# Performance work log

Hardware: AMD Instinct MI355X
Metric: run time of the kernel (lower is better)

## Reference

```python
import jax, jax.numpy as jnp
import numpy as np

N_HEADS = 16
LN_EPS = 1e-5


def setup_inputs() -> dict:
    key = jax.random.key(0)
    k_z, k_qkv, k_proj = jax.random.split(key, 3)
    b, n, dm = 4, 2048, 1024
    z = jax.random.normal(k_z, (b, n, dm), dtype=jnp.float32)
    gamma = jnp.ones((dm,), dtype=jnp.float32)
    beta = jnp.zeros((dm,), dtype=jnp.float32)
    # parameterize Linear weights as (in, out) so y = x @ w (same math as torch x @ W.T)
    w_qkv = jax.random.normal(k_qkv, (dm, 3 * dm), dtype=jnp.float32) * (1.0 / np.sqrt(dm))
    w_proj = jax.random.normal(k_proj, (dm, dm), dtype=jnp.float32) * (1.0 / np.sqrt(dm))
    b_proj = jnp.zeros((dm,), dtype=jnp.float32)
    return {"z": z, "gamma": gamma, "beta": beta, "w_qkv": w_qkv,
            "w_proj": w_proj, "b_proj": b_proj}


def reference(z, gamma, beta, w_qkv, w_proj, b_proj):
    b, n, dm = z.shape
    h = N_HEADS
    d = dm // h
    scaling = jnp.asarray(np.sqrt(dm / h), dtype=z.dtype)

    # LayerNorm over last dim
    mu = jnp.mean(z, axis=-1, keepdims=True)
    var = jnp.mean(jnp.square(z - mu), axis=-1, keepdims=True)
    zn = (z - mu) * jax.lax.rsqrt(var + LN_EPS) * gamma + beta

    qkv = zn @ w_qkv  # [b, n, 3*dm]
    # einops 'b n (h d qkv_n) -> qkv_n b h n d': qkv index is INNERMOST of packed dim
    qkv = qkv.reshape(b, n, h, d, 3)
    q = qkv[..., 0]  # [b, n, h, d]
    k = qkv[..., 1]
    v = qkv[..., 2]

    scores = jnp.einsum('bqhd,bkhd->bhqk', q, k) / scaling  # [b, h, n, n]
    att = jax.nn.softmax(scores, axis=-1)
    out = jnp.einsum('bhqk,bkhd->bqhd', att, v).reshape(b, n, dm)
    out = out @ w_proj + b_proj  # projection (drop_hidden=False); dropout is identity in eval
    return z + out
```

## Files before the change

kernel.cpp:

```cpp
#include <hip/hip_runtime.h>

typedef unsigned short ushort;
typedef unsigned int uint;

typedef __bf16 bf16x8 __attribute__((ext_vector_type(8)));
typedef float floatx4 __attribute__((ext_vector_type(4)));

constexpr int BATCH = 4;
constexpr int SEQ = 2048;
constexpr int DM = 1024;
constexpr int NH = 16;
constexpr int HD = 64;
constexpr int M = BATCH * SEQ;
constexpr int NQKV = 3 * DM;
constexpr float QSCALE = 0.18033688011112042f;

__device__ __forceinline__ ushort f2b(float f) {
    uint x; __builtin_memcpy(&x, &f, 4);
    x += 0x7fffu + ((x >> 16) & 1u);
    return (ushort)(x >> 16);
}

__device__ __forceinline__ void gload16(const ushort* g, ushort* l) {
    __builtin_amdgcn_global_load_lds(
        (const __attribute__((address_space(1))) void*)g,
        (__attribute__((address_space(3))) void*)l, 16, 0, 0);
}

__global__ __launch_bounds__(256) void transpose_cast(
    const float* __restrict__ in, ushort* __restrict__ out, int R, int C) {
    __shared__ ushort tile[64][65];
    int c0 = blockIdx.x * 64, r0 = blockIdx.y * 64;
    int tx = threadIdx.x & 63, ty = threadIdx.x >> 6;
#pragma unroll
    for (int i = 0; i < 64; i += 4)
        tile[i + ty][tx] = f2b(in[(size_t)(r0 + i + ty) * C + c0 + tx]);
    __syncthreads();
#pragma unroll
    for (int i = 0; i < 64; i += 4)
        out[(size_t)(c0 + i + ty) * R + r0 + tx] = tile[tx][i + ty];
}

__global__ __launch_bounds__(256) void ln_kernel(
    const float* __restrict__ z, const float* __restrict__ gamma,
    const float* __restrict__ beta, ushort* __restrict__ zn) {
    int row = blockIdx.x;
    int t = threadIdx.x;
    float4 v = reinterpret_cast<const float4*>(z + (size_t)row * DM)[t];
    float s = v.x + v.y + v.z + v.w;
    float sq = v.x * v.x + v.y * v.y + v.z * v.z + v.w * v.w;
#pragma unroll
    for (int off = 32; off >= 1; off >>= 1) {
        s  += __shfl_xor(s, off);
        sq += __shfl_xor(sq, off);
    }
    __shared__ float red[8];
    int wave = t >> 6;
    if ((t & 63) == 0) { red[wave] = s; red[wave + 4] = sq; }
    __syncthreads();
    s  = red[0] + red[1] + red[2] + red[3];
    sq = red[4] + red[5] + red[6] + red[7];
    float mean = s * (1.f / DM);
    float var  = sq * (1.f / DM) - mean * mean;
    float rstd = rsqrtf(var + 1e-5f);
    float4 g = reinterpret_cast<const float4*>(gamma)[t];
    float4 bt = reinterpret_cast<const float4*>(beta)[t];
    ushort4 o;
    o.x = f2b((v.x - mean) * rstd * g.x + bt.x);
    o.y = f2b((v.y - mean) * rstd * g.y + bt.y);
    o.z = f2b((v.z - mean) * rstd * g.z + bt.z);
    o.w = f2b((v.w - mean) * rstd * g.w + bt.w);
    reinterpret_cast<ushort4*>(zn + (size_t)row * DM)[t] = o;
}

__device__ __forceinline__ void gemm128_core(
    const ushort* __restrict__ A, const ushort* __restrict__ BT,
    int m0, int n0, int t, floatx4 (&acc)[4][4],
    ushort (*As)[32], ushort (*Bs)[32]) {
    int lane = t & 63, w = t >> 6;
    int l16 = lane & 15, quad = lane >> 4;
    int wm = (w >> 1) * 64, wn = (w & 1) * 64;
#pragma unroll
    for (int i = 0; i < 4; i++)
#pragma unroll
        for (int j = 0; j < 4; j++) acc[i][j] = (floatx4){0.f, 0.f, 0.f, 0.f};

    int sr = (w << 4) + (lane >> 2);
    int seg = (((lane & 3) ^ ((sr >> 1) & 3)) << 3);
    const ushort* gA0 = &A [(size_t)(m0 + sr) * DM + seg];
    const ushort* gA1 = &A [(size_t)(m0 + sr + 64) * DM + seg];
    const ushort* gB0 = &BT[(size_t)(n0 + sr) * DM + seg];
    const ushort* gB1 = &BT[(size_t)(n0 + sr + 64) * DM + seg];
    ushort* lA0 = &As[(w << 4)][0];
    ushort* lA1 = &As[64 + (w << 4)][0];
    ushort* lB0 = &Bs[(w << 4)][0];
    ushort* lB1 = &Bs[64 + (w << 4)][0];
    int sw = (l16 >> 1) & 3;

    for (int k0 = 0; k0 < DM; k0 += 32) {
        gload16(gA0 + k0, lA0);
        gload16(gA1 + k0, lA1);
        gload16(gB0 + k0, lB0);
        gload16(gB1 + k0, lB1);
        __syncthreads();
        bf16x8 af[4], bf[4];
#pragma unroll
        for (int i = 0; i < 4; i++)
            af[i] = *reinterpret_cast<const bf16x8*>(&As[wm + i * 16 + l16][(quad ^ sw) << 3]);
#pragma unroll
        for (int j = 0; j < 4; j++)
            bf[j] = *reinterpret_cast<const bf16x8*>(&Bs[wn + j * 16 + l16][(quad ^ sw) << 3]);
#pragma unroll
        for (int i = 0; i < 4; i++)
#pragma unroll
            for (int j = 0; j < 4; j++)
                acc[i][j] = __builtin_amdgcn_mfma_f32_16x16x32_bf16(af[i], bf[j], acc[i][j], 0, 0, 0);
        __syncthreads();
    }
}

__global__ __launch_bounds__(256) void gemm_qkv(
    const ushort* __restrict__ A,
    const ushort* __restrict__ BT,
    ushort* __restrict__ Q, ushort* __restrict__ K, ushort* __restrict__ V) {
    __shared__ ushort As[128][32];
    __shared__ ushort Bs[128][32];
    int t = threadIdx.x;
    int m0 = blockIdx.y * 128, n0 = blockIdx.x * 128;
    floatx4 acc[4][4];
    gemm128_core(A, BT, m0, n0, t, acc, As, Bs);
    int lane = t & 63, w = t >> 6;
    int l16 = lane & 15, quad = lane >> 4;
    int wm = (w >> 1) * 64, wn = (w & 1) * 64;
#pragma unroll
    for (int j = 0; j < 4; j++) {
        int col = n0 + wn + j * 16 + l16;
        int which = col % 3, hd = col / 3;
        int hi = hd >> 6, di = hd & 63;
        ushort* dst = (which == 0) ? Q : (which == 1) ? K : V;
        float scale = (which == 0) ? QSCALE : 1.0f;
#pragma unroll
        for (int i = 0; i < 4; i++) {
#pragma unroll
            for (int r = 0; r < 4; r++) {
                int row = m0 + wm + i * 16 + quad * 4 + r;
                int bb = row >> 11, nn = row & 2047;
                size_t idx = (which == 2)
                    ? ((size_t)(bb * NH + hi) * HD + di) * SEQ + nn
                    : ((size_t)(bb * NH + hi) * SEQ + nn) * HD + di;
                dst[idx] = f2b(acc[i][j][r] * scale);
            }
        }
    }
}

__global__ __launch_bounds__(256) void gemm_proj(
    const ushort* __restrict__ A,
    const ushort* __restrict__ BT,
    const float* __restrict__ bias, const float* __restrict__ z,
    float* __restrict__ out) {
    __shared__ ushort As[128][32];
    __shared__ ushort Bs[128][32];
    int t = threadIdx.x;
    int m0 = blockIdx.y * 128, n0 = blockIdx.x * 128;
    floatx4 acc[4][4];
    gemm128_core(A, BT, m0, n0, t, acc, As, Bs);
    int lane = t & 63, w = t >> 6;
    int l16 = lane & 15, quad = lane >> 4;
    int wm = (w >> 1) * 64, wn = (w & 1) * 64;
#pragma unroll
    for (int j = 0; j < 4; j++) {
        int col = n0 + wn + j * 16 + l16;
        float bz = bias[col];
#pragma unroll
        for (int i = 0; i < 4; i++) {
#pragma unroll
            for (int r = 0; r < 4; r++) {
                int row = m0 + wm + i * 16 + quad * 4 + r;
                out[(size_t)row * DM + col] =
                    acc[i][j][r] + bz + z[(size_t)row * DM + col];
            }
        }
    }
}

__global__ __launch_bounds__(256) void attn_kernel(
    const ushort* __restrict__ Q, const ushort* __restrict__ K,
    const ushort* __restrict__ Vt, ushort* __restrict__ O) {
    __shared__ ushort QsPs[64 * 64];
    __shared__ ushort Ks[2][64 * 64];
    __shared__ ushort Vs[2][64 * 64];
    int t = threadIdx.x;
    int lane = t & 63, w = t >> 6;
    int l16 = lane & 15, quad = lane >> 4;
    int bb = blockIdx.y >> 4, h = blockIdx.y & 15;
    int q0 = blockIdx.x * 64;
    const ushort* Qg = Q  + (size_t)((bb * NH + h) * SEQ + q0) * HD;
    const ushort* Kg = K  + (size_t)((bb * NH + h) * SEQ) * HD;
    const ushort* Vg = Vt + (size_t)((bb * NH + h) * HD) * SEQ;

    int srow = lane >> 3;
    int lseg = (lane & 7) ^ srow;
    int r0 = 8 * w + srow;

    gload16(Qg + (size_t)r0 * HD + lseg * 8,        &QsPs[w * 512]);
    gload16(Qg + (size_t)(32 + r0) * HD + lseg * 8, &QsPs[2048 + w * 512]);
    gload16(Kg + (size_t)r0 * HD + lseg * 8,        &Ks[0][w * 512]);
    gload16(Kg + (size_t)(32 + r0) * HD + lseg * 8, &Ks[0][2048 + w * 512]);
    gload16(Vg + (size_t)r0 * SEQ + lseg * 8,       &Vs[0][w * 512]);
    gload16(Vg + (size_t)(32 + r0) * SEQ + lseg * 8,&Vs[0][2048 + w * 512]);
    __syncthreads();

    int swl = l16 & 7;
    bf16x8 aq0 = *reinterpret_cast<const bf16x8*>(&QsPs[(16 * w + l16) * 64 + ((quad ^ swl) << 3)]);
    bf16x8 aq1 = *reinterpret_cast<const bf16x8*>(&QsPs[(16 * w + l16) * 64 + (((quad + 4) ^ swl) << 3)]);
    ushort* PsRow = &QsPs[(16 * w + l16) * 64];

    bf16x8 bones;
    {
        union { ushort u[8]; bf16x8 v; } cvt;
        ushort one = (l16 == 0) ? (ushort)0x3F80 : (ushort)0;
#pragma unroll
        for (int i = 0; i < 8; i++) cvt.u[i] = one;
        bones = cvt.v;
    }

    floatx4 Oacc[4], lacc = (floatx4){0.f, 0.f, 0.f, 0.f};
#pragma unroll
    for (int tt = 0; tt < 4; tt++) Oacc[tt] = (floatx4){0.f, 0.f, 0.f, 0.f};

    constexpr int NT = SEQ / 64;
    for (int kt = 0; kt < NT; kt++) {
        int cur = kt & 1;
        if (kt + 1 < NT) {
            const ushort* Kn = Kg + (size_t)(kt + 1) * 64 * HD;
            const ushort* Vn = Vg + (size_t)(kt + 1) * 64;
            gload16(Kn + (size_t)r0 * HD + lseg * 8,         &Ks[cur ^ 1][w * 512]);
            gload16(Kn + (size_t)(32 + r0) * HD + lseg * 8,  &Ks[cur ^ 1][2048 + w * 512]);
            gload16(Vn + (size_t)r0 * SEQ + lseg * 8,        &Vs[cur ^ 1][w * 512]);
            gload16(Vn + (size_t)(32 + r0) * SEQ + lseg * 8, &Vs[cur ^ 1][2048 + w * 512]);
        }
        const ushort* Kc = Ks[cur];
        const ushort* Vc = Vs[cur];

        floatx4 sacc[4];
#pragma unroll
        for (int nt = 0; nt < 4; nt++) {
            bf16x8 ak0 = *reinterpret_cast<const bf16x8*>(&Kc[(nt * 16 + l16) * 64 + ((quad ^ swl) << 3)]);
            bf16x8 ak1 = *reinterpret_cast<const bf16x8*>(&Kc[(nt * 16 + l16) * 64 + (((quad + 4) ^ swl) << 3)]);
            floatx4 sv = (floatx4){0.f, 0.f, 0.f, 0.f};
            sv = __builtin_amdgcn_mfma_f32_16x16x32_bf16(ak0, aq0, sv, 0, 0, 0);
            sv = __builtin_amdgcn_mfma_f32_16x16x32_bf16(ak1, aq1, sv, 0, 0, 0);
            sacc[nt] = sv;
        }
#pragma unroll
        for (int nt = 0; nt < 4; nt++) {
            float p0 = __builtin_amdgcn_exp2f(sacc[nt][0]);
            float p1 = __builtin_amdgcn_exp2f(sacc[nt][1]);
            float p2 = __builtin_amdgcn_exp2f(sacc[nt][2]);
            float p3 = __builtin_amdgcn_exp2f(sacc[nt][3]);
            uint b0, b1, b2, b3;
            __builtin_memcpy(&b0, &p0, 4); __builtin_memcpy(&b1, &p1, 4);
            __builtin_memcpy(&b2, &p2, 4); __builtin_memcpy(&b3, &p3, 4);
            uint2 pk;
            pk.x = __builtin_amdgcn_perm(b1, b0, 0x07060302u);
            pk.y = __builtin_amdgcn_perm(b3, b2, 0x07060302u);
            int lseg2 = 2 * nt + (quad >> 1);
            *reinterpret_cast<uint2*>(&PsRow[((lseg2 ^ swl) << 3) + (quad & 1) * 4]) = pk;
        }
#pragma unroll
        for (int ks = 0; ks < 2; ks++) {
            bf16x8 ap = *reinterpret_cast<const bf16x8*>(
                &PsRow[(((4 * ks + quad) ^ swl) << 3)]);
            lacc = __builtin_amdgcn_mfma_f32_16x16x32_bf16(ap, bones, lacc, 0, 0, 0);
#pragma unroll
            for (int tt = 0; tt < 4; tt++) {
                bf16x8 bv = *reinterpret_cast<const bf16x8*>(
                    &Vc[(tt * 16 + l16) * 64 + ((((ks * 4 + quad)) ^ swl) << 3)]);
                Oacc[tt] = __builtin_amdgcn_mfma_f32_16x16x32_bf16(ap, bv, Oacc[tt], 0, 0, 0);
            }
        }
        __syncthreads();
    }
    float lq[4];
#pragma unroll
    for (int j = 0; j < 4; j++) lq[j] = __shfl(lacc[j], quad << 4);

#pragma unroll
    for (int tt = 0; tt < 4; tt++) {
#pragma unroll
        for (int j = 0; j < 4; j++) {
            int n = q0 + w * 16 + quad * 4 + j;
            int dcol = tt * 16 + l16;
            float val = Oacc[tt][j] / lq[j];
            O[(size_t)(bb * SEQ + n) * DM + h * HD + dcol] = f2b(val);
        }
    }
}

extern "C" void kernel_launch(void* const* d_in, const int* in_sizes, int n_in,
                              void* d_out, int out_size, void* d_ws, size_t ws_size,
                              hipStream_t stream) {
    const float* z      = (const float*)d_in[0];
    const float* gamma  = (const float*)d_in[1];
    const float* beta   = (const float*)d_in[2];
    const float* w_qkv  = (const float*)d_in[3];
    const float* w_proj = (const float*)d_in[4];
    const float* b_proj = (const float*)d_in[5];
    float* out = (float*)d_out;

    char* ws = (char*)d_ws;
    const size_t SZ = (size_t)M * DM * sizeof(ushort);
    ushort* zn   = (ushort*)(ws);
    ushort* Qb   = (ushort*)(ws + SZ);
    ushort* Kb   = (ushort*)(ws + 2 * SZ);
    ushort* Vb   = (ushort*)(ws + 3 * SZ);
    ushort* wqT  = (ushort*)(ws + 4 * SZ);
    ushort* wpT  = (ushort*)(ws + 4 * SZ + (size_t)DM * NQKV * sizeof(ushort));
    ushort* Ob = zn;

    dim3 tq(NQKV / 64, DM / 64);
    transpose_cast<<<tq, 256, 0, stream>>>(w_qkv, wqT, DM, NQKV);
    dim3 tp(DM / 64, DM / 64);
    transpose_cast<<<tp, 256, 0, stream>>>(w_proj, wpT, DM, DM);
    ln_kernel<<<M, 256, 0, stream>>>(z, gamma, beta, zn);
    dim3 g1(NQKV / 128, M / 128);
    gemm_qkv<<<g1, 256, 0, stream>>>(zn, wqT, Qb, Kb, Vb);
    dim3 g2(SEQ / 64, BATCH * NH);
    attn_kernel<<<g2, 256, 0, stream>>>(Qb, Kb, Vb, Ob);
    dim3 g3(DM / 128, M / 128);
    gemm_proj<<<g3, 256, 0, stream>>>(Ob, wpT, b_proj, z, out);
}
```

Measured before the change: 327.4 us.

## Permute QKV weight columns so GEMM epilogue writes contiguous Q/K/V tiles via LDS

The QKV weight transpose now reorders output columns so all Q columns come first, then K, then V. Each 128-column GEMM tile therefore maps to a single tensor and a contiguous range of heads. The epilogue stages the accumulator tile in shared memory, transposing it for V, then writes 16-byte vectorized rows. This replaces the old scattered 2-byte stores with their per-element modulo/divide index math. The cost is extra LDS and two barrier-separated passes in the epilogue.

```diff
diff --git a/kernel.cpp b/kernel.cpp
--- a/kernel.cpp
+++ b/kernel.cpp
@@ -39,6 +39,23 @@
 #pragma unroll
     for (int i = 0; i < 64; i += 4)
         out[(size_t)(c0 + i + ty) * R + r0 + tx] = tile[tx][i + ty];
+}
+
+__global__ __launch_bounds__(256) void transpose_cast_qkv(
+    const float* __restrict__ in, ushort* __restrict__ out) {
+    __shared__ ushort tile[64][65];
+    int c0 = blockIdx.x * 64, r0 = blockIdx.y * 64;
+    int tx = threadIdx.x & 63, ty = threadIdx.x >> 6;
+#pragma unroll
+    for (int i = 0; i < 64; i += 4)
+        tile[i + ty][tx] = f2b(in[(size_t)(r0 + i + ty) * NQKV + c0 + tx]);
+    __syncthreads();
+#pragma unroll
+    for (int i = 0; i < 64; i += 4) {
+        int c = c0 + i + ty;
+        int cp = (c % 3) * DM + c / 3;
+        out[(size_t)cp * DM + r0 + tx] = tile[tx][i + ty];
+    }
 }
 
 __global__ __launch_bounds__(256) void ln_kernel(
@@ -125,6 +142,7 @@
     ushort* __restrict__ Q, ushort* __restrict__ K, ushort* __restrict__ V) {
     __shared__ ushort As[128][32];
     __shared__ ushort Bs[128][32];
+    __shared__ ushort Cs[9216];
     int t = threadIdx.x;
     int m0 = blockIdx.y * 128, n0 = blockIdx.x * 128;
     floatx4 acc[4][4];
@@ -132,23 +150,59 @@
     int lane = t & 63, w = t >> 6;
     int l16 = lane & 15, quad = lane >> 4;
     int wm = (w >> 1) * 64, wn = (w & 1) * 64;
-#pragma unroll
-    for (int j = 0; j < 4; j++) {
-        int col = n0 + wn + j * 16 + l16;
-        int which = col % 3, hd = col / 3;
-        int hi = hd >> 6, di = hd & 63;
-        ushort* dst = (which == 0) ? Q : (which == 1) ? K : V;
-        float scale = (which == 0) ? QSCALE : 1.0f;
-#pragma unroll
-        for (int i = 0; i < 4; i++) {
-#pragma unroll
-            for (int r = 0; r < 4; r++) {
-                int row = m0 + wm + i * 16 + quad * 4 + r;
-                int bb = row >> 11, nn = row & 2047;
-                size_t idx = (which == 2)
-                    ? ((size_t)(bb * NH + hi) * HD + di) * SEQ + nn
-                    : ((size_t)(bb * NH + hi) * SEQ + nn) * HD + di;
-                dst[idx] = f2b(acc[i][j][r] * scale);
+    int which = n0 >> 10;
+    int hd0 = n0 & 1023;
+    float scale = (which == 0) ? QSCALE : 1.0f;
+    int bb = m0 >> 11;
+    int nb = m0 & 2047;
+    ushort* dstQK = (which == 0) ? Q : K;
+
+#pragma unroll
+    for (int p = 0; p < 2; p++) {
+        __syncthreads();
+        if ((w >> 1) == p) {
+            if (which < 2) {
+#pragma unroll
+                for (int i = 0; i < 4; i++)
+#pragma unroll
+                    for (int j = 0; j < 4; j++)
+#pragma unroll
+                        for (int r = 0; r < 4; r++)
+                            Cs[(i * 16 + quad * 4 + r) * 136 + wn + j * 16 + l16] =
+                                f2b(acc[i][j][r] * scale);
+            } else {
+#pragma unroll
+                for (int i = 0; i < 4; i++)
+#pragma unroll
+                    for (int j = 0; j < 4; j++)
+#pragma unroll
+                        for (int r = 0; r < 4; r++)
+                            Cs[(wn + j * 16 + l16) * 72 + i * 16 + quad * 4 + r] =
+                                f2b(acc[i][j][r]);
+            }
+        }
+        __syncthreads();
+        if (which < 2) {
+            int ch = (t & 15) * 8;
+#pragma unroll
+            for (int u = 0; u < 4; u++) {
+                int lr = (t >> 4) + u * 16;
+                int n = nb + p * 64 + lr;
+                int hh = (hd0 + ch) >> 6, dd = ch & 63;
+                *reinterpret_cast<uint4*>(
+                    &dstQK[((size_t)((bb * NH + hh) * SEQ) + n) * HD + dd]) =
+                    *reinterpret_cast<const uint4*>(&Cs[lr * 136 + ch]);
+            }
+        } else {
+            int nch = (t & 7) * 8;
+#pragma unroll
+            for (int u = 0; u < 4; u++) {
+                int dc = (t >> 3) + u * 32;
+                int hh = (hd0 >> 6) + (dc >> 6), dd = dc & 63;
+                int n = nb + p * 64 + nch;
+                *reinterpret_cast<uint4*>(
+                    &V[((size_t)((bb * NH + hh) * HD) + dd) * SEQ + n]) =
+                    *reinterpret_cast<const uint4*>(&Cs[dc * 72 + nch]);
             }
         }
     }
@@ -320,7 +374,7 @@
     ushort* Ob = zn;
 
     dim3 tq(NQKV / 64, DM / 64);
-    transpose_cast<<<tq, 256, 0, stream>>>(w_qkv, wqT, DM, NQKV);
+    transpose_cast_qkv<<<tq, 256, 0, stream>>>(w_qkv, wqT);
     dim3 tp(DM / 64, DM / 64);
     transpose_cast<<<tp, 256, 0, stream>>>(w_proj, wpT, DM, DM);
     ln_kernel<<<M, 256, 0, stream>>>(z, gamma, beta, zn);
```

Result: faster. 312.9 us (-4.4%).
